# Optimization experiments

Measured on AMD Instinct MI355X. Metric: run time of the kernel, lower is better.

Reference implementation:

```python
import jax, jax.numpy as jnp
import numpy as np

WML, B, S, D = 64, 64, 40, 512  # word_max_len, batch, sents_max_len, dim


def setup_inputs() -> dict:
    key = jax.random.key(0)
    ks = jax.random.split(key, 8)
    source = jax.random.normal(ks[0], (B, D), dtype=jnp.float32)
    word_bank = jax.random.normal(ks[1], (WML, B, S, D), dtype=jnp.float32)
    # per-sentence word counts in [1, WML] so every sentence has >=1 valid token
    word_lengths = jax.random.randint(ks[2], (B, S), 1, WML + 1)
    sent_bank = jax.random.normal(ks[3], (S, B, D), dtype=jnp.float32)
    sent_lengths = jax.random.randint(ks[4], (B,), 1, S + 1)  # unused by forward math
    static_attn = jax.random.uniform(ks[5], (B, S), dtype=jnp.float32)
    scale = 1.0 / np.sqrt(D)
    W_word = jax.random.normal(ks[6], (D, D), dtype=jnp.float32) * scale
    W_sent = jax.random.normal(ks[7], (D, D), dtype=jnp.float32) * scale
    W_out = jax.random.normal(jax.random.fold_in(key, 99), (D, 2 * D), dtype=jnp.float32) * scale
    return {"source": source, "word_bank": word_bank, "word_lengths": word_lengths,
            "sent_bank": sent_bank, "sent_lengths": sent_lengths, "static_attn": static_attn,
            "W_word": W_word, "W_sent": W_sent, "W_out": W_out}


def reference(source, word_bank, word_lengths, sent_bank, sent_lengths, static_attn, W_word, W_sent, W_out):
    wml, batch, sents, dim = word_bank.shape
    # [wml, B, S, D] -> [B, S, wml, D] -> [B, S*wml, D]  (matches torch transpose chain)
    wb = jnp.transpose(word_bank, (1, 2, 0, 3)).reshape(batch, sents * wml, dim)
    # score(source, wb, 'word'): (source @ W_word^T) dotted with each word vector
    word_align = jnp.einsum('bd,bnd->bn', source @ W_word.T, wb)          # [B, S*wml]
    sb = jnp.transpose(sent_bank, (1, 0, 2))                               # [B, S, D]
    sent_align = jnp.einsum('bd,bsd->bs', source @ W_sent.T, sb)          # [B, S]
    # triple product: word score * sentence score * static attention
    align = (word_align.reshape(batch, sents, wml)
             * (sent_align * static_attn)[:, :, None]).reshape(batch, sents * wml)
    # sequence mask per sentence, flattened to [B, S*wml]
    mask = (jnp.arange(wml)[None, None, :] < word_lengths[:, :, None]).reshape(batch, sents * wml)
    align = jnp.where(mask, align, -jnp.inf)
    align_vectors = jax.nn.softmax(align, axis=-1) + 1e-20               # [B, S*wml]
    c = jnp.einsum('bn,bnd->bd', align_vectors, wb)                       # [B, D]
    attn_h = jnp.tanh(jnp.concatenate([c, source], axis=-1) @ W_out.T)    # [B, D]
    return attn_h, align_vectors
```

## Files before the change

### kernel.cpp

```cpp
#include <hip/hip_runtime.h>
#include <math.h>

#define BB   64
#define SS   40
#define WMLC 64
#define DD   512
#define NN   2560
#define NBLK 20
#define WPB  4
#define NWAVES (NBLK*WPB)
#define RPW (NN/NWAVES)
#define L2E 1.4426950408889634f

__device__ __forceinline__ float wave_reduce_sum(float v) {
    #pragma unroll
    for (int off = 32; off > 0; off >>= 1) v += __shfl_xor(v, off, 64);
    return v;
}

__global__ __launch_bounds__(256) void k_proj(const float* __restrict__ src,
                                              const float* __restrict__ Ww,
                                              const float* __restrict__ Ws,
                                              float* __restrict__ qw,
                                              float* __restrict__ qs) {
    __shared__ float xs[DD];
    const int b = blockIdx.y;
    const int t = threadIdx.x;
    const float* W = blockIdx.x ? Ws : Ww;
    float* q = blockIdx.x ? qs : qw;
    ((float2*)xs)[t] = ((const float2*)(src + b * DD))[t];
    __syncthreads();
    const float* r0 = W + (size_t)t * DD;
    const float* r1 = W + (size_t)(t + 256) * DD;
    float acc0 = 0.f, acc1 = 0.f;
    for (int k = 0; k < DD; k += 4) {
        float4 x  = *(const float4*)(xs + k);
        float4 w0 = *(const float4*)(r0 + k);
        float4 w1 = *(const float4*)(r1 + k);
        acc0 += x.x * w0.x + x.y * w0.y + x.z * w0.z + x.w * w0.w;
        acc1 += x.x * w1.x + x.y * w1.y + x.z * w1.z + x.w * w1.w;
    }
    q[b * DD + t] = acc0;
    q[b * DD + t + 256] = acc1;
}

__global__ __launch_bounds__(256) void k_sstat(const float* __restrict__ qs,
                                               const float* __restrict__ sb,
                                               const float* __restrict__ sa,
                                               float* __restrict__ sstat) {
    const int b = blockIdx.x;
    const int t = threadIdx.x, wave = t >> 6, lane = t & 63;
    const int d0 = lane * 4, d1 = 256 + lane * 4;
    const float4 q0 = *(const float4*)(qs + b * DD + d0);
    const float4 q1 = *(const float4*)(qs + b * DD + d1);
    for (int j = 0; j < SS / WPB; ++j) {
        const int s = wave * (SS / WPB) + j;
        const float* row = sb + ((size_t)s * BB + b) * DD;
        float4 a0 = *(const float4*)(row + d0);
        float4 a1 = *(const float4*)(row + d1);
        float p = a0.x * q0.x + a0.y * q0.y + a0.z * q0.z + a0.w * q0.w
                + a1.x * q1.x + a1.y * q1.y + a1.z * q1.z + a1.w * q1.w;
        p = wave_reduce_sum(p);
        if (lane == 0) sstat[b * SS + s] = p * sa[b * SS + s];
    }
}

__global__ __launch_bounds__(256) void k_main(const float* __restrict__ wb,
                                              const float* __restrict__ qw,
                                              const float* __restrict__ sstat,
                                              const int* __restrict__ wl,
                                              float* __restrict__ scores,
                                              float* __restrict__ part_c,
                                              float* __restrict__ part_ml) {
    const int b = blockIdx.y;
    const int chunk = blockIdx.x;
    const int t = threadIdx.x, wave = t >> 6, lane = t & 63;
    const int gw = chunk * WPB + wave;
    const int d0 = lane * 4, d1 = 256 + lane * 4;
    const float4 q0 = *(const float4*)(qw + b * DD + d0);
    const float4 q1 = *(const float4*)(qw + b * DD + d1);

    float m = -INFINITY, l = 0.f;
    float4 c0 = {0.f, 0.f, 0.f, 0.f}, c1 = {0.f, 0.f, 0.f, 0.f};

    for (int k = 0; k < RPW; ++k) {
        const int n = gw + k * NWAVES;
        const int s = n >> 6, w = n & 63;
        if (w >= wl[b * SS + s]) continue;
        const float* row = wb + (size_t)(((w * BB + b) * SS + s)) * DD;
        float4 a0 = *(const float4*)(row + d0);
        float4 a1 = *(const float4*)(row + d1);
        float p = a0.x * q0.x + a0.y * q0.y + a0.z * q0.z + a0.w * q0.w
                + a1.x * q1.x + a1.y * q1.y + a1.z * q1.z + a1.w * q1.w;
        p = wave_reduce_sum(p);
        const float a = p * sstat[b * SS + s];
        if (lane == 0) scores[b * NN + n] = a;
        if (a > m) {
            const float sc = (m == -INFINITY) ? 0.f : exp2f((m - a) * L2E);
            l *= sc;
            c0.x *= sc; c0.y *= sc; c0.z *= sc; c0.w *= sc;
            c1.x *= sc; c1.y *= sc; c1.z *= sc; c1.w *= sc;
            m = a;
        }
        const float e = exp2f((a - m) * L2E);
        l += e;
        c0.x += e * a0.x; c0.y += e * a0.y; c0.z += e * a0.z; c0.w += e * a0.w;
        c1.x += e * a1.x; c1.y += e * a1.y; c1.z += e * a1.z; c1.w += e * a1.w;
    }

    __shared__ float s_m[WPB], s_l[WPB];
    __shared__ float s_c[WPB][DD];
    *(float4*)(&s_c[wave][d0]) = c0;
    *(float4*)(&s_c[wave][d1]) = c1;
    if (lane == 0) { s_m[wave] = m; s_l[wave] = l; }
    __syncthreads();
    const float mb = fmaxf(fmaxf(s_m[0], s_m[1]), fmaxf(s_m[2], s_m[3]));
    float lb = 0.f, cA = 0.f, cB = 0.f;
    #pragma unroll
    for (int wv = 0; wv < WPB; ++wv) {
        const float mi = s_m[wv];
        const float sc = (mi == -INFINITY) ? 0.f : exp2f((mi - mb) * L2E);
        lb += s_l[wv] * sc;
        cA += s_c[wv][t] * sc;
        cB += s_c[wv][t + 256] * sc;
    }
    const int pidx = b * NBLK + chunk;
    part_c[(size_t)pidx * DD + t] = cA;
    part_c[(size_t)pidx * DD + t + 256] = cB;
    if (t == 0) { part_ml[pidx * 2] = mb; part_ml[pidx * 2 + 1] = lb; }
}

__global__ __launch_bounds__(256) void k_reduce(const float* __restrict__ part_c,
                                                const float* __restrict__ part_ml,
                                                float* __restrict__ c_final,
                                                float* __restrict__ mz) {
    const int b = blockIdx.x, t = threadIdx.x;
    float mg = -INFINITY;
    for (int i = 0; i < NBLK; ++i) mg = fmaxf(mg, part_ml[(b * NBLK + i) * 2]);
    float Z = 0.f, cA = 0.f, cB = 0.f;
    for (int i = 0; i < NBLK; ++i) {
        const float mi = part_ml[(b * NBLK + i) * 2];
        const float li = part_ml[(b * NBLK + i) * 2 + 1];
        const float sc = (mi == -INFINITY) ? 0.f : exp2f((mi - mg) * L2E);
        Z += li * sc;
        cA += part_c[(size_t)(b * NBLK + i) * DD + t] * sc;
        cB += part_c[(size_t)(b * NBLK + i) * DD + t + 256] * sc;
    }
    const float invZ = 1.0f / Z;
    c_final[b * DD + t] = cA * invZ;
    c_final[b * DD + t + 256] = cB * invZ;
    if (t == 0) { mz[b * 2] = mg; mz[b * 2 + 1] = invZ; }
}

__global__ __launch_bounds__(256) void k_align(const int* __restrict__ wl,
                                               const float* __restrict__ mz,
                                               float* __restrict__ av) {
    const int b = blockIdx.y;
    const int n = blockIdx.x * 256 + threadIdx.x;
    const int s = n >> 6, w = n & 63;
    const int len = wl[b * SS + s];
    float v = 1e-20f;
    if (w < len) {
        const float a = av[b * NN + n];
        v = exp2f((a - mz[b * 2]) * L2E) * mz[b * 2 + 1] + 1e-20f;
    }
    av[b * NN + n] = v;
}

__global__ __launch_bounds__(256) void k_attnh(const float* __restrict__ c_final,
                                               const float* __restrict__ src,
                                               const float* __restrict__ Wout,
                                               float* __restrict__ out) {
    __shared__ float xs[2 * DD];
    const int b = blockIdx.y, t = threadIdx.x;
    ((float2*)xs)[t] = ((const float2*)(c_final + b * DD))[t];
    ((float2*)(xs + DD))[t] = ((const float2*)(src + b * DD))[t];
    __syncthreads();
    const int d = blockIdx.x * 256 + t;
    const float* row = Wout + (size_t)d * (2 * DD);
    float acc = 0.f;
    for (int k = 0; k < 2 * DD; k += 4) {
        float4 x = *(const float4*)(xs + k);
        float4 w = *(const float4*)(row + k);
        acc += x.x * w.x + x.y * w.y + x.z * w.z + x.w * w.w;
    }
    out[b * DD + d] = tanhf(acc);
}

extern "C" void kernel_launch(void* const* d_in, const int* in_sizes, int n_in,
                              void* d_out, int out_size, void* d_ws, size_t ws_size,
                              hipStream_t stream) {
    const float* src = (const float*)d_in[0];
    const float* wb  = (const float*)d_in[1];
    const int*   wl  = (const int*)  d_in[2];
    const float* sb  = (const float*)d_in[3];
    const float* sa  = (const float*)d_in[5];
    const float* Ww  = (const float*)d_in[6];
    const float* Wsn = (const float*)d_in[7];
    const float* Wo  = (const float*)d_in[8];
    float* out = (float*)d_out;

    float* ws = (float*)d_ws;
    float* qw      = ws;
    float* qs      = ws + 32768;
    float* sstat   = ws + 65536;
    float* part_c  = ws + 68096;
    float* part_ml = ws + 723456;
    float* mz      = ws + 726016;
    float* c_final = ws + 726144;

    float* scores = out + BB * DD;

    hipLaunchKernelGGL(k_proj,   dim3(2, BB),       dim3(256), 0, stream, src, Ww, Wsn, qw, qs);
    hipLaunchKernelGGL(k_sstat,  dim3(BB),          dim3(256), 0, stream, qs, sb, sa, sstat);
    hipLaunchKernelGGL(k_main,   dim3(NBLK, BB),    dim3(256), 0, stream, wb, qw, sstat, wl,
                       scores, part_c, part_ml);
    hipLaunchKernelGGL(k_reduce, dim3(BB),          dim3(256), 0, stream, part_c, part_ml, c_final, mz);
    hipLaunchKernelGGL(k_align,  dim3(NN / 256, BB), dim3(256), 0, stream, wl, mz, scores);
    hipLaunchKernelGGL(k_attnh,  dim3(2, BB),       dim3(256), 0, stream, c_final, src, Wo, out);
}
```

Measured before the change: 517.8 us.

## Fuse projection kernels and post-processing kernels, unroll main loop by two

```diff
diff --git a/kernel.cpp b/kernel.cpp
--- a/kernel.cpp
+++ b/kernel.cpp
@@ -18,41 +18,46 @@
     return v;
 }
 
-__global__ __launch_bounds__(256) void k_proj(const float* __restrict__ src,
-                                              const float* __restrict__ Ww,
-                                              const float* __restrict__ Ws,
-                                              float* __restrict__ qw,
-                                              float* __restrict__ qs) {
+__global__ __launch_bounds__(256) void k_pre(const float* __restrict__ src,
+                                             const float* __restrict__ Ww,
+                                             const float* __restrict__ Ws,
+                                             const float* __restrict__ sb,
+                                             const float* __restrict__ sa,
+                                             float* __restrict__ qw,
+                                             float* __restrict__ sstat) {
     __shared__ float xs[DD];
-    const int b = blockIdx.y;
+    __shared__ float qss[DD];
+    const int b = blockIdx.x;
     const int t = threadIdx.x;
-    const float* W = blockIdx.x ? Ws : Ww;
-    float* q = blockIdx.x ? qs : qw;
     ((float2*)xs)[t] = ((const float2*)(src + b * DD))[t];
     __syncthreads();
-    const float* r0 = W + (size_t)t * DD;
-    const float* r1 = W + (size_t)(t + 256) * DD;
-    float acc0 = 0.f, acc1 = 0.f;
+
+    const float* ww0 = Ww + (size_t)t * DD;
+    const float* ww1 = Ww + (size_t)(t + 256) * DD;
+    const float* ws0 = Ws + (size_t)t * DD;
+    const float* ws1 = Ws + (size_t)(t + 256) * DD;
+    float aw0 = 0.f, aw1 = 0.f, as0 = 0.f, as1 = 0.f;
     for (int k = 0; k < DD; k += 4) {
-        float4 x  = *(const float4*)(xs + k);
-        float4 w0 = *(const float4*)(r0 + k);
-        float4 w1 = *(const float4*)(r1 + k);
-        acc0 += x.x * w0.x + x.y * w0.y + x.z * w0.z + x.w * w0.w;
-        acc1 += x.x * w1.x + x.y * w1.y + x.z * w1.z + x.w * w1.w;
-    }
-    q[b * DD + t] = acc0;
-    q[b * DD + t + 256] = acc1;
-}
-
-__global__ __launch_bounds__(256) void k_sstat(const float* __restrict__ qs,
-                                               const float* __restrict__ sb,
-                                               const float* __restrict__ sa,
-                                               float* __restrict__ sstat) {
-    const int b = blockIdx.x;
-    const int t = threadIdx.x, wave = t >> 6, lane = t & 63;
+        float4 x = *(const float4*)(xs + k);
+        float4 w0 = *(const float4*)(ww0 + k);
+        float4 w1 = *(const float4*)(ww1 + k);
+        float4 s0 = *(const float4*)(ws0 + k);
+        float4 s1 = *(const float4*)(ws1 + k);
+        aw0 += x.x * w0.x + x.y * w0.y + x.z * w0.z + x.w * w0.w;
+        aw1 += x.x * w1.x + x.y * w1.y + x.z * w1.z + x.w * w1.w;
+        as0 += x.x * s0.x + x.y * s0.y + x.z * s0.z + x.w * s0.w;
+        as1 += x.x * s1.x + x.y * s1.y + x.z * s1.z + x.w * s1.w;
+    }
+    qw[b * DD + t] = aw0;
+    qw[b * DD + t + 256] = aw1;
+    qss[t] = as0;
+    qss[t + 256] = as1;
+    __syncthreads();
+
+    const int wave = t >> 6, lane = t & 63;
     const int d0 = lane * 4, d1 = 256 + lane * 4;
-    const float4 q0 = *(const float4*)(qs + b * DD + d0);
-    const float4 q1 = *(const float4*)(qs + b * DD + d1);
+    const float4 q0 = *(const float4*)(qss + d0);
+    const float4 q1 = *(const float4*)(qss + d1);
     for (int j = 0; j < SS / WPB; ++j) {
         const int s = wave * (SS / WPB) + j;
         const float* row = sb + ((size_t)s * BB + b) * DD;
@@ -83,29 +88,58 @@
     float m = -INFINITY, l = 0.f;
     float4 c0 = {0.f, 0.f, 0.f, 0.f}, c1 = {0.f, 0.f, 0.f, 0.f};
 
-    for (int k = 0; k < RPW; ++k) {
-        const int n = gw + k * NWAVES;
-        const int s = n >> 6, w = n & 63;
-        if (w >= wl[b * SS + s]) continue;
-        const float* row = wb + (size_t)(((w * BB + b) * SS + s)) * DD;
-        float4 a0 = *(const float4*)(row + d0);
-        float4 a1 = *(const float4*)(row + d1);
-        float p = a0.x * q0.x + a0.y * q0.y + a0.z * q0.z + a0.w * q0.w
-                + a1.x * q1.x + a1.y * q1.y + a1.z * q1.z + a1.w * q1.w;
-        p = wave_reduce_sum(p);
-        const float a = p * sstat[b * SS + s];
-        if (lane == 0) scores[b * NN + n] = a;
-        if (a > m) {
-            const float sc = (m == -INFINITY) ? 0.f : exp2f((m - a) * L2E);
-            l *= sc;
-            c0.x *= sc; c0.y *= sc; c0.z *= sc; c0.w *= sc;
-            c1.x *= sc; c1.y *= sc; c1.z *= sc; c1.w *= sc;
-            m = a;
-        }
-        const float e = exp2f((a - m) * L2E);
-        l += e;
-        c0.x += e * a0.x; c0.y += e * a0.y; c0.z += e * a0.z; c0.w += e * a0.w;
-        c1.x += e * a1.x; c1.y += e * a1.y; c1.z += e * a1.z; c1.w += e * a1.w;
+    for (int k = 0; k < RPW; k += 2) {
+        const int n0 = gw + k * NWAVES;
+        const int n1 = n0 + NWAVES;
+        const int s0 = n0 >> 6, w0 = n0 & 63;
+        const int s1 = n1 >> 6, w1 = n1 & 63;
+        const bool v0 = (w0 < wl[b * SS + s0]);
+        const bool v1 = (w1 < wl[b * SS + s1]);
+        float4 a00, a01, a10, a11;
+        float p0 = 0.f, p1 = 0.f;
+        const float* r0 = wb + (size_t)(((w0 * BB + b) * SS + s0)) * DD;
+        const float* r1 = wb + (size_t)(((w1 * BB + b) * SS + s1)) * DD;
+        if (v0) { a00 = *(const float4*)(r0 + d0); a01 = *(const float4*)(r0 + d1); }
+        if (v1) { a10 = *(const float4*)(r1 + d0); a11 = *(const float4*)(r1 + d1); }
+        if (v0) p0 = a00.x * q0.x + a00.y * q0.y + a00.z * q0.z + a00.w * q0.w
+                   + a01.x * q1.x + a01.y * q1.y + a01.z * q1.z + a01.w * q1.w;
+        if (v1) p1 = a10.x * q0.x + a10.y * q0.y + a10.z * q0.z + a10.w * q0.w
+                   + a11.x * q1.x + a11.y * q1.y + a11.z * q1.z + a11.w * q1.w;
+        #pragma unroll
+        for (int off = 32; off > 0; off >>= 1) {
+            p0 += __shfl_xor(p0, off, 64);
+            p1 += __shfl_xor(p1, off, 64);
+        }
+        if (v0) {
+            const float a = p0 * sstat[b * SS + s0];
+            if (lane == 0) scores[b * NN + n0] = a;
+            if (a > m) {
+                const float sc = (m == -INFINITY) ? 0.f : exp2f((m - a) * L2E);
+                l *= sc;
+                c0.x *= sc; c0.y *= sc; c0.z *= sc; c0.w *= sc;
+                c1.x *= sc; c1.y *= sc; c1.z *= sc; c1.w *= sc;
+                m = a;
+            }
+            const float e = exp2f((a - m) * L2E);
+            l += e;
+            c0.x += e * a00.x; c0.y += e * a00.y; c0.z += e * a00.z; c0.w += e * a00.w;
+            c1.x += e * a01.x; c1.y += e * a01.y; c1.z += e * a01.z; c1.w += e * a01.w;
+        }
+        if (v1) {
+            const float a = p1 * sstat[b * SS + s1];
+            if (lane == 0) scores[b * NN + n1] = a;
+            if (a > m) {
+                const float sc = (m == -INFINITY) ? 0.f : exp2f((m - a) * L2E);
+                l *= sc;
+                c0.x *= sc; c0.y *= sc; c0.z *= sc; c0.w *= sc;
+                c1.x *= sc; c1.y *= sc; c1.z *= sc; c1.w *= sc;
+                m = a;
+            }
+            const float e = exp2f((a - m) * L2E);
+            l += e;
+            c0.x += e * a10.x; c0.y += e * a10.y; c0.z += e * a10.z; c0.w += e * a10.w;
+            c1.x += e * a11.x; c1.y += e * a11.y; c1.z += e * a11.z; c1.w += e * a11.w;
+        }
     }
 
     __shared__ float s_m[WPB], s_l[WPB];
@@ -130,12 +164,17 @@
     if (t == 0) { part_ml[pidx * 2] = mb; part_ml[pidx * 2 + 1] = lb; }
 }
 
-__global__ __launch_bounds__(256) void k_reduce(const float* __restrict__ part_c,
-                                                const float* __restrict__ part_ml,
-                                                float* __restrict__ c_final,
-                                                float* __restrict__ mz) {
+__global__ __launch_bounds__(256) void k_post(const float* __restrict__ part_c,
+                                              const float* __restrict__ part_ml,
+                                              const int* __restrict__ wl,
+                                              const float* __restrict__ src,
+                                              const float* __restrict__ Wout,
+                                              float* __restrict__ out) {
+    __shared__ float xs[2 * DD];
     const int b = blockIdx.x, t = threadIdx.x;
+
     float mg = -INFINITY;
+    #pragma unroll
     for (int i = 0; i < NBLK; ++i) mg = fmaxf(mg, part_ml[(b * NBLK + i) * 2]);
     float Z = 0.f, cA = 0.f, cB = 0.f;
     for (int i = 0; i < NBLK; ++i) {
@@ -147,44 +186,34 @@
         cB += part_c[(size_t)(b * NBLK + i) * DD + t + 256] * sc;
     }
     const float invZ = 1.0f / Z;
-    c_final[b * DD + t] = cA * invZ;
-    c_final[b * DD + t + 256] = cB * invZ;
-    if (t == 0) { mz[b * 2] = mg; mz[b * 2 + 1] = invZ; }
-}
-
-__global__ __launch_bounds__(256) void k_align(const int* __restrict__ wl,
-                                               const float* __restrict__ mz,
-                                               float* __restrict__ av) {
-    const int b = blockIdx.y;
-    const int n = blockIdx.x * 256 + threadIdx.x;
-    const int s = n >> 6, w = n & 63;
-    const int len = wl[b * SS + s];
-    float v = 1e-20f;
-    if (w < len) {
-        const float a = av[b * NN + n];
-        v = exp2f((a - mz[b * 2]) * L2E) * mz[b * 2 + 1] + 1e-20f;
-    }
-    av[b * NN + n] = v;
-}
-
-__global__ __launch_bounds__(256) void k_attnh(const float* __restrict__ c_final,
-                                               const float* __restrict__ src,
-                                               const float* __restrict__ Wout,
-                                               float* __restrict__ out) {
-    __shared__ float xs[2 * DD];
-    const int b = blockIdx.y, t = threadIdx.x;
-    ((float2*)xs)[t] = ((const float2*)(c_final + b * DD))[t];
-    ((float2*)(xs + DD))[t] = ((const float2*)(src + b * DD))[t];
-    __syncthreads();
-    const int d = blockIdx.x * 256 + t;
-    const float* row = Wout + (size_t)d * (2 * DD);
-    float acc = 0.f;
-    for (int k = 0; k < 2 * DD; k += 4) {
-        float4 x = *(const float4*)(xs + k);
-        float4 w = *(const float4*)(row + k);
-        acc += x.x * w.x + x.y * w.y + x.z * w.z + x.w * w.w;
-    }
-    out[b * DD + d] = tanhf(acc);
+    xs[t] = cA * invZ;
+    xs[t + 256] = cB * invZ;
+    xs[DD + t] = src[b * DD + t];
+    xs[DD + t + 256] = src[b * DD + t + 256];
+    __syncthreads();
+
+    float* av = out + BB * DD + (size_t)b * NN;
+    #pragma unroll
+    for (int j = 0; j < NN / 256; ++j) {
+        const int n = j * 256 + t;
+        const int s = n >> 6, w = n & 63;
+        float v = 1e-20f;
+        if (w < wl[b * SS + s]) v = exp2f((av[n] - mg) * L2E) * invZ + 1e-20f;
+        av[n] = v;
+    }
+
+    #pragma unroll
+    for (int rep = 0; rep < 2; ++rep) {
+        const int d = rep * 256 + t;
+        const float* row = Wout + (size_t)d * (2 * DD);
+        float acc = 0.f;
+        for (int k = 0; k < 2 * DD; k += 4) {
+            float4 x = *(const float4*)(xs + k);
+            float4 w = *(const float4*)(row + k);
+            acc += x.x * w.x + x.y * w.y + x.z * w.z + x.w * w.w;
+        }
+        out[b * DD + d] = tanhf(acc);
+    }
 }
 
 extern "C" void kernel_launch(void* const* d_in, const int* in_sizes, int n_in,
@@ -202,20 +231,14 @@
 
     float* ws = (float*)d_ws;
     float* qw      = ws;
-    float* qs      = ws + 32768;
-    float* sstat   = ws + 65536;
-    float* part_c  = ws + 68096;
-    float* part_ml = ws + 723456;
-    float* mz      = ws + 726016;
-    float* c_final = ws + 726144;
+    float* sstat   = ws + 32768;
+    float* part_c  = ws + 35328;
+    float* part_ml = ws + 690688;
 
     float* scores = out + BB * DD;
 
-    hipLaunchKernelGGL(k_proj,   dim3(2, BB),       dim3(256), 0, stream, src, Ww, Wsn, qw, qs);
-    hipLaunchKernelGGL(k_sstat,  dim3(BB),          dim3(256), 0, stream, qs, sb, sa, sstat);
-    hipLaunchKernelGGL(k_main,   dim3(NBLK, BB),    dim3(256), 0, stream, wb, qw, sstat, wl,
+    hipLaunchKernelGGL(k_pre,  dim3(BB),       dim3(256), 0, stream, src, Ww, Wsn, sb, sa, qw, sstat);
+    hipLaunchKernelGGL(k_main, dim3(NBLK, BB), dim3(256), 0, stream, wb, qw, sstat, wl,
                        scores, part_c, part_ml);
-    hipLaunchKernelGGL(k_reduce, dim3(BB),          dim3(256), 0, stream, part_c, part_ml, c_final, mz);
-    hipLaunchKernelGGL(k_align,  dim3(NN / 256, BB), dim3(256), 0, stream, wl, mz, scores);
-    hipLaunchKernelGGL(k_attnh,  dim3(2, BB),       dim3(256), 0, stream, c_final, src, Wo, out);
-}
+    hipLaunchKernelGGL(k_post, dim3(BB),       dim3(256), 0, stream, part_c, part_ml, wl, src, Wo, out);
+}
```

New measurement: 580.2 us. 1.12x slower.
